# Kernel tuning notes

Measured on AMD Instinct MI355X. Metric: run time of the kernel, lower is better.

Reference implementation:

```python
import jax, jax.numpy as jnp
import numpy as np

MAX_ITER = 10   # float32 branch of cg()
TOL = 1e-10

def _cdot(a, b):
    # complex_dot: sum(conj(a) * b) over all elements
    return jnp.sum(jnp.conj(a) * b)

def _A(p, smaps, mask):
    # p: [H,W] complex, smaps: [C,H,W] complex, mask: [H,W] real
    return jnp.fft.fft2(smaps * p[None], norm='ortho') * mask[None]

def _AH(y, smaps, mask):
    imgs = jnp.fft.ifft2(y * mask[None], norm='ortho')
    return jnp.sum(jnp.conj(smaps) * imgs, axis=0)  # [H,W]

def _cg(M, rhs):
    # conjugate gradient, faithful to the TF while_loop body
    def cond(s):
        i, rTr, x, r, p = s
        return jnp.logical_and(i < MAX_ITER, rTr > TOL)
    def body(s):
        i, rTr, x, r, p = s
        Ap = M(p)
        alpha = rTr / jnp.real(_cdot(p, Ap))
        x = x + p * alpha
        r = r - Ap * alpha
        rTrNew = jnp.real(_cdot(r, r))
        beta = rTrNew / rTr
        p = r + p * beta
        return (i + 1, rTrNew, x, r, p)
    rTr0 = jnp.real(_cdot(rhs, rhs))
    s0 = (jnp.int32(0), rTr0, jnp.zeros_like(rhs), rhs, rhs)
    return jax.lax.while_loop(cond, body, s0)[2]

def _solve_one(lambdaa, rhs, smaps, mask):
    M = lambda p: _AH(_A(p, smaps, mask), smaps, mask) + p * lambdaa
    return _cg(M, rhs)

_solve_b = jax.vmap(_solve_one, in_axes=(None, 0, 0, 0))  # replaces map_fn
_AH_b = jax.vmap(_AH, in_axes=(0, 0, 0))

def setup_inputs():
    key = jax.random.key(0)
    ks = jax.random.split(key, 7)
    B, C, H, W = 4, 16, 384, 384
    f = lambda k, s: jax.random.normal(k, s, dtype=jnp.float32)
    return {
        'lambdaa': 0.05 * jnp.ones((), jnp.float32),
        'x_re': f(ks[0], (B, H, W)),
        'x_im': f(ks[1], (B, H, W)),
        'y_re': f(ks[2], (B, C, H, W)),
        'y_im': f(ks[3], (B, C, H, W)),
        'smaps_re': f(ks[4], (B, C, H, W)),
        'smaps_im': f(ks[5], (B, C, H, W)),
        'mask': (jax.random.uniform(ks[6], (B, H, W)) < 0.33).astype(jnp.float32),
    }

def reference(lambdaa, x_re, x_im, y_re, y_im, smaps_re, smaps_im, mask):
    x = jax.lax.complex(x_re, x_im)
    y = jax.lax.complex(y_re, y_im)
    smaps = jax.lax.complex(smaps_re, smaps_im)
    # rhs = AH(y) + lambdaa * x
    rhs = _AH_b(y, smaps, mask) + x * lambdaa
    out = _solve_b(lambdaa, rhs, smaps, mask)  # [B,H,W] complex
    return jnp.stack([out.real, out.imag], axis=-1)  # [B,H,W,2] float32
```

## Files before the change

kernel.cpp:

```cpp
#include <hip/hip_runtime.h>
#include <hip/hip_fp16.h>


#define Bn 4
#define Cn 16
#define Hn 384
#define Wn 384
#define NPIX (Hn*Wn)
#define NPIX2 (NPIX/2)
#define TPB 256
#define CTPB 512
#define NCOL 16
#define TOLF 1e-10f
#define NITER 10
#define RED_BLKS 72
#define GRP 4
#define CPG 4
#define RPITCH 416
#define CPITCH 417

__device__ __forceinline__ float2 cadd(float2 a, float2 b){ return make_float2(a.x+b.x, a.y+b.y); }
__device__ __forceinline__ float2 csub(float2 a, float2 b){ return make_float2(a.x-b.x, a.y-b.y); }
__device__ __forceinline__ float2 cmulf(float2 a, float2 b){
  return make_float2(a.x*b.x - a.y*b.y, a.x*b.y + a.y*b.x);
}

__device__ __forceinline__ void wave_fence(){ asm volatile("s_waitcnt lgkmcnt(0)" ::: "memory"); }

template<int IMM>
__device__ __forceinline__ float2 shx(float2 v){
  int x = __builtin_amdgcn_ds_swizzle(__float_as_int(v.x), IMM);
  int y = __builtin_amdgcn_ds_swizzle(__float_as_int(v.y), IMM);
  return make_float2(__int_as_float(x), __int_as_float(y));
}

template<int CTRL>
__device__ __forceinline__ float2 dpp2(float2 v){
  int x = __builtin_amdgcn_mov_dpp(__float_as_int(v.x), CTRL, 0xF, 0xF, true);
  int y = __builtin_amdgcn_mov_dpp(__float_as_int(v.y), CTRL, 0xF, 0xF, true);
  return make_float2(__int_as_float(x), __int_as_float(y));
}
__device__ __forceinline__ float2 xchg1 (float2 v){ return dpp2<0xB1>(v);  }
__device__ __forceinline__ float2 xchg2 (float2 v){ return dpp2<0x4E>(v);  }
__device__ __forceinline__ float2 xchg4 (float2 v){ return dpp2<0x1B>(dpp2<0x141>(v)); }
__device__ __forceinline__ float2 xchg8 (float2 v){ return dpp2<0x128>(v); }
__device__ __forceinline__ float2 xchg16(float2 v){ return shx<0x401F>(v); }

__device__ __forceinline__ int rev5(int x){
  return ((x&1)<<4) | ((x&2)<<2) | (x&4) | ((x&8)>>2) | ((x&16)>>4);
}

__device__ __forceinline__ int offmap(int w){ return w + ((w*683)>>13); }

template<int DIR>
__device__ __forceinline__ void fft12(float2* v)
{
  const float S3 = (DIR<0) ? -0.86602540378443864676f : 0.86602540378443864676f;
  const float sg = (DIR<0) ? -1.f : 1.f;
  float2 t[4][3];
#pragma unroll
  for (int b = 0; b < 4; ++b) {
    float2 a0 = v[b], a1 = v[4+b], a2 = v[8+b];
    float2 s = cadd(a1,a2), d = csub(a1,a2);
    float2 mm = make_float2(a0.x - 0.5f*s.x, a0.y - 0.5f*s.y);
    float2 e  = make_float2(-d.y*S3, d.x*S3);
    t[b][0] = cadd(a0,s);
    t[b][1] = cadd(mm,e);
    t[b][2] = csub(mm,e);
  }
  const float2 w1  = make_float2(0.86602540378443864676f, sg*0.5f);
  const float2 w2  = make_float2(0.5f, sg*0.86602540378443864676f);
  const float2 w3  = make_float2(0.f, sg);
  const float2 w4t = make_float2(-0.5f, sg*0.86602540378443864676f);
  const float2 w6  = make_float2(-1.f, 0.f);
  t[1][1] = cmulf(t[1][1], w1);  t[1][2] = cmulf(t[1][2], w2);
  t[2][1] = cmulf(t[2][1], w2);  t[2][2] = cmulf(t[2][2], w4t);
  t[3][1] = cmulf(t[3][1], w3);  t[3][2] = cmulf(t[3][2], w6);
#pragma unroll
  for (int c = 0; c < 3; ++c) {
    float2 e = cadd(t[0][c], t[2][c]);
    float2 f = csub(t[0][c], t[2][c]);
    float2 g = cadd(t[1][c], t[3][c]);
    float2 h = csub(t[1][c], t[3][c]);
    float2 ih = (DIR<0) ? make_float2(h.y, -h.x) : make_float2(-h.y, h.x);
    v[c]   = cadd(e,g);
    v[c+3] = cadd(f,ih);
    v[c+6] = csub(e,g);
    v[c+9] = csub(f,ih);
  }
}

template<int DIR>
__device__ __forceinline__ void fft32_lanes(float2* v, int li)
{
  const float c2pi = (DIR<0) ? -6.2831853071795864769f : 6.2831853071795864769f;
  const float sg   = (DIR<0) ? -1.f : 1.f;
  float s, c;
  __sincosf(c2pi*(1.f/32.f)*(float)(li&15), &s, &c); float2 wA = make_float2(c,s);
  __sincosf(c2pi*(1.f/16.f)*(float)(li&7),  &s, &c); float2 wB = make_float2(c,s);
  __sincosf(c2pi*(1.f/ 8.f)*(float)(li&3),  &s, &c); float2 wC = make_float2(c,s);
  bool bA = li & 16, bB = li & 8, bC = li & 4, bD = li & 2, bE = li & 1;
#pragma unroll
  for (int k = 0; k < 12; ++k) {
    float2 a = v[k], o;
    o = xchg16(a); a = bA ? cmulf(csub(o,a), wA) : cadd(a,o);
    o = xchg8 (a); a = bB ? cmulf(csub(o,a), wB) : cadd(a,o);
    o = xchg4 (a); a = bC ? cmulf(csub(o,a), wC) : cadd(a,o);
    o = xchg2 (a);
    { float2 su = cadd(a,o), d = csub(o,a);
      float2 dw = bE ? make_float2(-sg*d.y, sg*d.x) : d;
      a = bD ? dw : su; }
    o = xchg1 (a); a = bE ? csub(o,a) : cadd(a,o);
    v[k] = a;
  }
}

template<int DIR>
__device__ __forceinline__ void fft32_lanes_dit(float2* v, int li)
{
  const float c2pi = (DIR<0) ? -6.2831853071795864769f : 6.2831853071795864769f;
  const float sg   = (DIR<0) ? -1.f : 1.f;
  float s, c;
  __sincosf(c2pi*(1.f/32.f)*(float)(li&15), &s, &c); float2 wA = make_float2(c,s);
  __sincosf(c2pi*(1.f/16.f)*(float)(li&7),  &s, &c); float2 wB = make_float2(c,s);
  __sincosf(c2pi*(1.f/ 8.f)*(float)(li&3),  &s, &c); float2 wC = make_float2(c,s);
  bool bA = li & 16, bB = li & 8, bC = li & 4, bD = li & 2, bE = li & 1;
#pragma unroll
  for (int k = 0; k < 12; ++k) {
    float2 a = v[k], o;
    o = xchg1(a); a = bE ? csub(o,a) : cadd(a,o);
    { float2 aw = make_float2(-sg*a.y, sg*a.x);
      a = (bD && bE) ? aw : a;
      o = xchg2(a); a = bD ? csub(o,a) : cadd(a,o); }
    { float2 aw = cmulf(a, wC); a = bC ? aw : a;
      o = xchg4(a); a = bC ? csub(o,a) : cadd(a,o); }
    { float2 aw = cmulf(a, wB); a = bB ? aw : a;
      o = xchg8(a); a = bB ? csub(o,a) : cadd(a,o); }
    { float2 aw = cmulf(a, wA); a = bA ? aw : a;
      o = xchg16(a); a = bA ? csub(o,a) : cadd(a,o); }
    v[k] = a;
  }
}

template<int DIR>
__device__ __forceinline__ void fft384(float2* v, int li)
{
  fft12<DIR>(v);
  const float c2pi = (DIR<0) ? -6.2831853071795864769f : 6.2831853071795864769f;
  float s, c;
  __sincosf(c2pi*(1.f/384.f)*(float)li, &s, &c);
  float2 W = make_float2(c,s), cw = W;
#pragma unroll
  for (int k = 1; k < 12; ++k) { v[k] = cmulf(v[k], cw); cw = cmulf(cw, W); }
  fft32_lanes<DIR>(v, li);
}

template<int DIR>
__device__ __forceinline__ void fft384_scr(float2* v, int li)
{
  fft32_lanes_dit<DIR>(v, li);
  const float c2pi = (DIR<0) ? -6.2831853071795864769f : 6.2831853071795864769f;
  float s, c;
  __sincosf(c2pi*(1.f/384.f)*(float)li, &s, &c);
  float2 W = make_float2(c,s), cw = W;
#pragma unroll
  for (int k = 1; k < 12; ++k) { v[k] = cmulf(v[k], cw); cw = cmulf(cw, W); }
  fft12<DIR>(v);
}


template<bool HS>
__global__ __launch_bounds__(TPB) void k_row_fwd(
    const float2* __restrict__ p, const float* __restrict__ Sre,
    const float* __restrict__ Sim, const __half2* __restrict__ Sh,
    __half2* __restrict__ tmp)
{
  int tid = threadIdx.x;
  int wave = tid>>6, lane = tid&63, sub = lane>>5, li = lane&31;
  int row = wave*2 + sub;
  int tile = blockIdx.x % (Hn/8);
  int bc   = blockIdx.x / (Hn/8);
  int b = bc / Cn;
  int h = tile*8 + row;
  size_t gbase = (size_t)bc*NPIX + (size_t)h*Wn;
  size_t pbase = (size_t)b*NPIX + (size_t)h*Wn;

  float2 v[12];
#pragma unroll
  for (int k = 0; k < 12; ++k) {
    int w = 32*k + li;
    float2 pv = p[pbase + w];
    float sr, si;
    if (HS) { float2 sv = __half22float2(Sh[gbase + w]); sr = sv.x; si = sv.y; }
    else    { sr = Sre[gbase + w]; si = Sim[gbase + w]; }
    v[k] = make_float2(sr*pv.x - si*pv.y, sr*pv.y + si*pv.x);
  }
  fft384<-1>(v, li);
#pragma unroll
  for (int k = 0; k < 12; ++k)
    tmp[gbase + 32*k + li] = __float22half2_rn(v[k]);
}

template<bool HS>
__global__ __launch_bounds__(TPB) void k_row_inv_scr(
    const __half2* __restrict__ tmp, const float* __restrict__ Sre,
    const float* __restrict__ Sim, const __half2* __restrict__ Sh,
    float2* __restrict__ partial)
{
  int tid = threadIdx.x;
  int wave = tid>>6, lane = tid&63, sub = lane>>5, li = lane&31;
  int row = wave*2 + sub;
  int tile = blockIdx.x % (Hn/8);
  int rest = blockIdx.x / (Hn/8);
  int g = rest % GRP;
  int b = rest / GRP;
  int h = tile*8 + row;

  size_t gbase0 = ((size_t)b*Cn + g*CPG)*NPIX + (size_t)h*Wn;
  __half2 hb[12];
#pragma unroll
  for (int k = 0; k < 12; ++k) hb[k] = tmp[gbase0 + 32*k + li];

  float2 acc[12];
#pragma unroll
  for (int k = 0; k < 12; ++k) acc[k] = make_float2(0.f, 0.f);

  for (int j = 0; j < CPG; ++j) {
    size_t gb = gbase0 + (size_t)j*NPIX;
    float2 vc[12];
#pragma unroll
    for (int k = 0; k < 12; ++k) vc[k] = __half22float2(hb[k]);
    if (j + 1 < CPG) {
      size_t gbn = gb + NPIX;
#pragma unroll
      for (int k = 0; k < 12; ++k) hb[k] = tmp[gbn + 32*k + li];
    }
    fft384_scr<1>(vc, li);
#pragma unroll
    for (int k = 0; k < 12; ++k) {
      int w = 32*k + li;
      float sr, si;
      if (HS) { float2 sv = __half22float2(Sh[gb + w]); sr = sv.x; si = sv.y; }
      else    { sr = Sre[gb + w]; si = Sim[gb + w]; }
      acc[k].x += sr*vc[k].x + si*vc[k].y;
      acc[k].y += sr*vc[k].y - si*vc[k].x;
    }
  }
  size_t pbase = ((size_t)g*Bn + b)*NPIX + (size_t)h*Wn;
#pragma unroll
  for (int k = 0; k < 12; ++k) partial[pbase + 32*k + li] = acc[k];
}

__global__ __launch_bounds__(TPB) void k_row_inv_nat(
    const __half2* __restrict__ tmp, const float* __restrict__ Sre,
    const float* __restrict__ Sim, float2* __restrict__ partial)
{
  __shared__ float2 lbuf[8*RPITCH];
  int tid = threadIdx.x;
  int wave = tid>>6, lane = tid&63, sub = lane>>5, li = lane&31;
  int row = wave*2 + sub;
  int tile = blockIdx.x % (Hn/8);
  int rest = blockIdx.x / (Hn/8);
  int g = rest % GRP;
  int b = rest / GRP;
  int h = tile*8 + row;
  int m = rev5(li);
  float2* lrow = lbuf + row*RPITCH;

  size_t gbase0 = ((size_t)b*Cn + g*CPG)*NPIX + (size_t)h*Wn;
  __half2 hb[12];
#pragma unroll
  for (int k = 0; k < 12; ++k) hb[k] = tmp[gbase0 + 32*k + li];

  float2 acc[12];
#pragma unroll
  for (int k = 0; k < 12; ++k) acc[k] = make_float2(0.f, 0.f);

  for (int j = 0; j < CPG; ++j) {
    size_t gb = gbase0 + (size_t)j*NPIX;
    float2 vc[12];
#pragma unroll
    for (int k = 0; k < 12; ++k) vc[k] = __half22float2(hb[k]);
    if (j + 1 < CPG) {
      size_t gbn = gb + NPIX;
#pragma unroll
      for (int k = 0; k < 12; ++k) hb[k] = tmp[gbn + 32*k + li];
    }
    fft384<1>(vc, li);
    wave_fence();
#pragma unroll
    for (int k = 0; k < 12; ++k) lrow[13*m + k] = vc[k];
    wave_fence();
#pragma unroll
    for (int k = 0; k < 12; ++k) {
      int w = 32*k + li;
      float2 u = lrow[offmap(w)];
      float sr = Sre[gb + w], si = Sim[gb + w];
      acc[k].x += sr*u.x + si*u.y;
      acc[k].y += sr*u.y - si*u.x;
    }
  }
  size_t pbase = ((size_t)g*Bn + b)*NPIX + (size_t)h*Wn;
#pragma unroll
  for (int k = 0; k < 12; ++k) partial[pbase + 32*k + li] = acc[k];
}

__global__ __launch_bounds__(TPB) void k_spack(
    const float* __restrict__ sre, const float* __restrict__ sim,
    __half2* __restrict__ sh)
{
  size_t i = (size_t)blockIdx.x*TPB + threadIdx.x;
  if (i < (size_t)Bn*Cn*NPIX) sh[i] = __floats2half2_rn(sre[i], sim[i]);
}

__global__ __launch_bounds__(TPB) void k_maskp(
    const float* __restrict__ mask, float* __restrict__ maskP,
    float* __restrict__ scal)
{
  int idx = blockIdx.x*TPB + threadIdx.x;
  if (blockIdx.x == 0) scal[threadIdx.x] = 0.0f;
  if (idx >= Bn*NPIX) return;
  int k = idx % 12; int t = idx / 12;
  int li = t & 31; t >>= 5;
  int wa = t % Wn; int b = t / Wn;
  int wt = (wa >> 5) + 12*rev5(wa & 31);
  maskP[idx] = mask[((size_t)b*Hn + (k + 12*rev5(li)))*Wn + wt] * (1.0f/(float)NPIX);
}

__global__ __launch_bounds__(CTPB) void k_col_full(
    __half2* __restrict__ tmp, const float* __restrict__ maskP)
{
  __shared__ __half2 dbuf[NCOL*CPITCH];
  int tid = threadIdx.x;
  int wave = tid>>6, lane = tid&63, sub = lane>>5, li = lane&31;
  int col = wave*2 + sub;
  int tile = blockIdx.x % (Wn/NCOL);
  int bc   = blockIdx.x / (Wn/NCOL);
  int b = bc / Cn;
  int w0 = tile*NCOL;
  size_t tbase = (size_t)bc*NPIX;

  for (int e = tid; e < NCOL*Hn; e += CTPB) {
    int wi = e & (NCOL-1), h = e >> 4;
    dbuf[wi*CPITCH + offmap(h)] = tmp[tbase + (size_t)h*Wn + w0 + wi];
  }
  __syncthreads();

  __half2* drow = dbuf + col*CPITCH;
  int w = w0 + col;
  const float4* mp4 = (const float4*)(maskP + (((size_t)b*Wn + w)*32 + li)*12);
  float4 m0 = mp4[0], m1 = mp4[1], m2 = mp4[2];
  float2 v[12];
#pragma unroll
  for (int k = 0; k < 12; ++k) v[k] = __half22float2(drow[offmap(32*k + li)]);
  fft384<-1>(v, li);
  float mk[12] = {m0.x,m0.y,m0.z,m0.w, m1.x,m1.y,m1.z,m1.w, m2.x,m2.y,m2.z,m2.w};
#pragma unroll
  for (int k = 0; k < 12; ++k) v[k] = make_float2(v[k].x*mk[k], v[k].y*mk[k]);
  fft384_scr<1>(v, li);
#pragma unroll
  for (int k = 0; k < 12; ++k) drow[offmap(32*k + li)] = __float22half2_rn(v[k]);
  __syncthreads();

  for (int e = tid; e < NCOL*Hn; e += CTPB) {
    int wi = e & (NCOL-1), h = e >> 4;
    tmp[tbase + (size_t)h*Wn + w0 + wi] = dbuf[wi*CPITCH + offmap(h)];
  }
}

__global__ __launch_bounds__(CTPB) void k_col_rhs(
    const float* __restrict__ yre, const float* __restrict__ yim,
    const float* __restrict__ mask, __half2* __restrict__ tmp)
{
  __shared__ float2 dbuf[NCOL*CPITCH];
  int tid = threadIdx.x;
  int wave = tid>>6, lane = tid&63, sub = lane>>5, li = lane&31;
  int col = wave*2 + sub;
  int tile = blockIdx.x % (Wn/NCOL);
  int bc   = blockIdx.x / (Wn/NCOL);
  int b = bc / Cn;
  int w0 = tile*NCOL;
  size_t tbase = (size_t)bc*NPIX;
  size_t mbase = (size_t)b*NPIX;

  for (int e = tid; e < NCOL*Hn; e += CTPB) {
    int wi = e & (NCOL-1), h = e >> 4;
    size_t gi = (size_t)h*Wn + w0 + wi;
    float mv = mask[mbase + gi] * (1.0f/384.0f);
    dbuf[wi*CPITCH + offmap(h)] = make_float2(yre[tbase+gi]*mv, yim[tbase+gi]*mv);
  }
  __syncthreads();

  float2* drow = dbuf + col*CPITCH;
  int m = rev5(li);
  float2 v[12];
#pragma unroll
  for (int k = 0; k < 12; ++k) v[k] = drow[offmap(32*k + li)];
  fft384<1>(v, li);
  wave_fence();
#pragma unroll
  for (int k = 0; k < 12; ++k) drow[13*m + k] = v[k];
  __syncthreads();

  for (int e = tid; e < NCOL*Hn; e += CTPB) {
    int wi = e & (NCOL-1), h = e >> 4;
    tmp[tbase + (size_t)h*Wn + w0 + wi] = __float22half2_rn(dbuf[wi*CPITCH + offmap(h)]);
  }
}


__device__ __forceinline__ void block_reduce_atomic(float sum, float* target)
{
  __shared__ float red[TPB/64];
  for (int off = 32; off > 0; off >>= 1) sum += __shfl_down(sum, off, 64);
  int wv = threadIdx.x >> 6;
  if ((threadIdx.x & 63) == 0) red[wv] = sum;
  __syncthreads();
  if (threadIdx.x == 0) {
    float t = red[0] + red[1] + red[2] + red[3];
    unsafeAtomicAdd(target, t);
  }
  __syncthreads();
}

__global__ __launch_bounds__(TPB) void k_rhs_init(
    const float* __restrict__ xre, const float* __restrict__ xim,
    const float* __restrict__ lam, const float2* __restrict__ partial,
    float2* __restrict__ r, float2* __restrict__ p, float2* __restrict__ x,
    float* __restrict__ scal)
{
  int b = blockIdx.y;
  float l = lam[0];
  float sum = 0.0f;
  const float2* xr2 = (const float2*)(xre + (size_t)b*NPIX);
  const float2* xi2 = (const float2*)(xim + (size_t)b*NPIX);
  float4* r4 = (float4*)(r + (size_t)b*NPIX);
  float4* p4 = (float4*)(p + (size_t)b*NPIX);
  float4* x4 = (float4*)(x + (size_t)b*NPIX);
  for (int i = blockIdx.x*TPB + threadIdx.x; i < NPIX2; i += RED_BLKS*TPB) {
    float2 re = xr2[i], im = xi2[i];
    float4 rv = make_float4(l*re.x, l*im.x, l*re.y, l*im.y);
#pragma unroll
    for (int g = 0; g < GRP; ++g) {
      float4 pv = ((const float4*)(partial + ((size_t)g*Bn + b)*NPIX))[i];
      rv.x += pv.x; rv.y += pv.y; rv.z += pv.z; rv.w += pv.w;
    }
    r4[i] = rv; p4[i] = rv;
    x4[i] = make_float4(0.f, 0.f, 0.f, 0.f);
    sum += rv.x*rv.x + rv.y*rv.y + rv.z*rv.z + rv.w*rv.w;
  }
  block_reduce_atomic(sum, &scal[b]);
}

__global__ __launch_bounds__(TPB) void k_combine_dot3(
    const float2* __restrict__ p, const float2* __restrict__ r,
    const float* __restrict__ lam, const float2* __restrict__ partial,
    float2* __restrict__ Ap, float* __restrict__ slot)
{
  int b = blockIdx.y;
  float l = lam[0];
  float s_pAp = 0.f, s_AA = 0.f, s_rA = 0.f;
  const float4* p4 = (const float4*)(p + (size_t)b*NPIX);
  const float4* r4 = (const float4*)(r + (size_t)b*NPIX);
  float4* A4 = (float4*)(Ap + (size_t)b*NPIX);
  for (int i = blockIdx.x*TPB + threadIdx.x; i < NPIX2; i += RED_BLKS*TPB) {
    float4 pv = p4[i];
    float4 av = make_float4(l*pv.x, l*pv.y, l*pv.z, l*pv.w);
#pragma unroll
    for (int g = 0; g < GRP; ++g) {
      float4 qv = ((const float4*)(partial + ((size_t)g*Bn + b)*NPIX))[i];
      av.x += qv.x; av.y += qv.y; av.z += qv.z; av.w += qv.w;
    }
    A4[i] = av;
    float4 rv = r4[i];
    s_pAp += pv.x*av.x + pv.y*av.y + pv.z*av.z + pv.w*av.w;
    s_AA  += av.x*av.x + av.y*av.y + av.z*av.z + av.w*av.w;
    s_rA  += rv.x*av.x + rv.y*av.y + rv.z*av.z + rv.w*av.w;
  }
  block_reduce_atomic(s_pAp, &slot[b]);
  block_reduce_atomic(s_AA,  &slot[4+b]);
  block_reduce_atomic(s_rA,  &slot[8+b]);
}

__global__ __launch_bounds__(TPB) void k_upd(
    float2* __restrict__ x, float2* __restrict__ r, float2* __restrict__ p,
    const float2* __restrict__ Ap, float* __restrict__ scal, int it)
{
  int b = blockIdx.y;
  float rtr = scal[it*4 + b];
  const float* slot = scal + 64 + it*12;
  bool act = rtr > TOLF;
  float alpha = act ? rtr / slot[b] : 0.f;
  float rtrn = act ? fmaxf(rtr - 2.f*alpha*slot[8+b] + alpha*alpha*slot[4+b], 0.f) : rtr;
  float beta = act ? rtrn / rtr : 0.f;
  if (blockIdx.x == 0 && threadIdx.x == 0) scal[(it+1)*4 + b] = rtrn;
  if (!act) return;
  float4* x4 = (float4*)(x + (size_t)b*NPIX);
  float4* r4 = (float4*)(r + (size_t)b*NPIX);
  float4* p4 = (float4*)(p + (size_t)b*NPIX);
  const float4* A4 = (const float4*)(Ap + (size_t)b*NPIX);
  for (int i = blockIdx.x*TPB + threadIdx.x; i < NPIX2; i += RED_BLKS*TPB) {
    float4 pv = p4[i], av = A4[i], xv = x4[i], rv = r4[i];
    xv.x += alpha*pv.x; xv.y += alpha*pv.y; xv.z += alpha*pv.z; xv.w += alpha*pv.w;
    rv.x -= alpha*av.x; rv.y -= alpha*av.y; rv.z -= alpha*av.z; rv.w -= alpha*av.w;
    x4[i] = xv; r4[i] = rv;
    p4[i] = make_float4(rv.x + beta*pv.x, rv.y + beta*pv.y,
                        rv.z + beta*pv.z, rv.w + beta*pv.w);
  }
}


extern "C" void kernel_launch(void* const* d_in, const int* in_sizes, int n_in,
                              void* d_out, int out_size, void* d_ws, size_t ws_size,
                              hipStream_t stream)
{
  const float* lam  = (const float*)d_in[0];
  const float* xre  = (const float*)d_in[1];
  const float* xim  = (const float*)d_in[2];
  const float* yre  = (const float*)d_in[3];
  const float* yim  = (const float*)d_in[4];
  const float* sre  = (const float*)d_in[5];
  const float* sim  = (const float*)d_in[6];
  const float* mask = (const float*)d_in[7];

  const size_t szTmp  = (size_t)Bn*Cn*NPIX*sizeof(__half2);
  const size_t szVec  = (size_t)Bn*NPIX*sizeof(float2);
  const size_t szMask = (size_t)Bn*NPIX*sizeof(float);
  const size_t szSh   = (size_t)Bn*Cn*NPIX*sizeof(__half2);
  const size_t base   = szTmp + (size_t)GRP*szVec + 3*szVec + 2048 + szMask;
  const bool useSh    = (ws_size >= base + szSh);

  char* ws = (char*)d_ws;
  __half2* tmp = (__half2*)ws;  ws += szTmp;
  float2* part = (float2*)ws;   ws += (size_t)GRP*szVec;
  float2* r    = (float2*)ws;   ws += szVec;
  float2* p    = (float2*)ws;   ws += szVec;
  float2* Ap   = (float2*)ws;   ws += szVec;
  float*  scal = (float*)ws;    ws += 2048;
  float*  mskP = (float*)ws;    ws += szMask;
  __half2* Sh  = (__half2*)ws;
  float2* x    = (float2*)d_out;

  dim3 blk(TPB);
  dim3 rg(RED_BLKS, Bn);
  int grid_row = Bn*Cn*(Hn/8);
  int grid_col = Bn*Cn*(Wn/NCOL);
  int grid_inv = Bn*GRP*(Hn/8);

  k_maskp<<<(Bn*NPIX)/TPB, blk, 0, stream>>>(mask, mskP, scal);
  if (useSh)
    k_spack<<<(Bn*Cn*NPIX)/TPB, blk, 0, stream>>>(sre, sim, Sh);

  k_col_rhs<<<grid_col, CTPB, 0, stream>>>(yre, yim, mask, tmp);
  k_row_inv_nat<<<grid_inv, blk, 0, stream>>>(tmp, sre, sim, part);
  k_rhs_init<<<rg, blk, 0, stream>>>(xre, xim, lam, part, r, p, x, scal);

  for (int it = 0; it < NITER; ++it) {
    if (useSh) {
      k_row_fwd<true><<<grid_row, blk, 0, stream>>>(p, sre, sim, Sh, tmp);
      k_col_full<<<grid_col, CTPB, 0, stream>>>(tmp, mskP);
      k_row_inv_scr<true><<<grid_inv, blk, 0, stream>>>(tmp, sre, sim, Sh, part);
    } else {
      k_row_fwd<false><<<grid_row, blk, 0, stream>>>(p, sre, sim, Sh, tmp);
      k_col_full<<<grid_col, CTPB, 0, stream>>>(tmp, mskP);
      k_row_inv_scr<false><<<grid_inv, blk, 0, stream>>>(tmp, sre, sim, Sh, part);
    }
    k_combine_dot3<<<rg, blk, 0, stream>>>(p, r, lam, part, Ap, scal + 64 + it*12);
    k_upd<<<rg, blk, 0, stream>>>(x, r, p, Ap, scal, it);
  }
}
```

Before: 1.393 ms.

## Fuse CG vector update into next iteration's forward row FFT with ping-pong buffers

Removes the separate k_upd pass by recomputing alpha/beta and applying the r/p/x update inside the forward row FFT kernel of the next iteration, with only channel-0 blocks writing the updated vectors. New r and p go to ping-pong buffers so other channel blocks can still read the old values. A final k_upd_x kernel applies the last x update. In exchange, every channel block now reads Ap, r and p, and the path only runs when the workspace is large enough for the extra buffers.

```diff
diff --git a/kernel.cpp b/kernel.cpp
--- a/kernel.cpp
+++ b/kernel.cpp
@@ -194,6 +194,61 @@
     if (HS) { float2 sv = __half22float2(Sh[gbase + w]); sr = sv.x; si = sv.y; }
     else    { sr = Sre[gbase + w]; si = Sim[gbase + w]; }
     v[k] = make_float2(sr*pv.x - si*pv.y, sr*pv.y + si*pv.x);
+  }
+  fft384<-1>(v, li);
+#pragma unroll
+  for (int k = 0; k < 12; ++k)
+    tmp[gbase + 32*k + li] = __float22half2_rn(v[k]);
+}
+
+template<bool HS>
+__global__ __launch_bounds__(TPB) void k_row_fwd_upd(
+    const float2* __restrict__ pin, const float2* __restrict__ rin,
+    const float2* __restrict__ Ap, float* __restrict__ scal, int uidx,
+    float2* __restrict__ pout, float2* __restrict__ rout,
+    float2* __restrict__ x,
+    const float* __restrict__ Sre, const float* __restrict__ Sim,
+    const __half2* __restrict__ Sh, __half2* __restrict__ tmp)
+{
+  int tid = threadIdx.x;
+  int wave = tid>>6, lane = tid&63, sub = lane>>5, li = lane&31;
+  int row = wave*2 + sub;
+  int tile = blockIdx.x % (Hn/8);
+  int bc   = blockIdx.x / (Hn/8);
+  int b = bc / Cn;
+  int c = bc % Cn;
+  int h = tile*8 + row;
+  size_t gbase = (size_t)bc*NPIX + (size_t)h*Wn;
+  size_t pbase = (size_t)b*NPIX + (size_t)h*Wn;
+
+  float rtr = scal[uidx*4 + b];
+  const float* slot = scal + 64 + uidx*12;
+  bool act = rtr > TOLF;
+  float alpha = act ? rtr / slot[b] : 0.f;
+  float rtrn = act ? fmaxf(rtr - 2.f*alpha*slot[8+b] + alpha*alpha*slot[4+b], 0.f) : rtr;
+  float beta = act ? rtrn / rtr : 0.f;
+  if (c == 0 && tile == 0 && tid == 0) scal[(uidx+1)*4 + b] = rtrn;
+  bool wr = (c == 0);
+
+  float2 v[12];
+#pragma unroll
+  for (int k = 0; k < 12; ++k) {
+    int w = 32*k + li;
+    float2 pv = pin[pbase + w];
+    float2 av = Ap[pbase + w];
+    float2 rv = rin[pbase + w];
+    float2 rn = make_float2(rv.x - alpha*av.x, rv.y - alpha*av.y);
+    float2 pn = act ? make_float2(rn.x + beta*pv.x, rn.y + beta*pv.y) : pv;
+    if (wr) {
+      rout[pbase + w] = rn;
+      pout[pbase + w] = pn;
+      float2 xv = x[pbase + w];
+      x[pbase + w] = make_float2(xv.x + alpha*pv.x, xv.y + alpha*pv.y);
+    }
+    float sr, si;
+    if (HS) { float2 sv = __half22float2(Sh[gbase + w]); sr = sv.x; si = sv.y; }
+    else    { sr = Sre[gbase + w]; si = Sim[gbase + w]; }
+    v[k] = make_float2(sr*pn.x - si*pn.y, sr*pn.y + si*pn.x);
   }
   fft384<-1>(v, li);
 #pragma unroll
@@ -509,6 +564,25 @@
   }
 }
 
+__global__ __launch_bounds__(TPB) void k_upd_x(
+    float2* __restrict__ x, const float2* __restrict__ p,
+    const float* __restrict__ scal, int uidx)
+{
+  int b = blockIdx.y;
+  float rtr = scal[uidx*4 + b];
+  const float* slot = scal + 64 + uidx*12;
+  bool act = rtr > TOLF;
+  if (!act) return;
+  float alpha = rtr / slot[b];
+  float4* x4 = (float4*)(x + (size_t)b*NPIX);
+  const float4* p4 = (const float4*)(p + (size_t)b*NPIX);
+  for (int i = blockIdx.x*TPB + threadIdx.x; i < NPIX2; i += RED_BLKS*TPB) {
+    float4 pv = p4[i], xv = x4[i];
+    x4[i] = make_float4(xv.x + alpha*pv.x, xv.y + alpha*pv.y,
+                        xv.z + alpha*pv.z, xv.w + alpha*pv.w);
+  }
+}
+
 
 extern "C" void kernel_launch(void* const* d_in, const int* in_sizes, int n_in,
                               void* d_out, int out_size, void* d_ws, size_t ws_size,
@@ -529,16 +603,19 @@
   const size_t szSh   = (size_t)Bn*Cn*NPIX*sizeof(__half2);
   const size_t base   = szTmp + (size_t)GRP*szVec + 3*szVec + 2048 + szMask;
   const bool useSh    = (ws_size >= base + szSh);
+  const bool useFused = useSh && (ws_size >= base + szSh + 2*szVec);
 
   char* ws = (char*)d_ws;
   __half2* tmp = (__half2*)ws;  ws += szTmp;
   float2* part = (float2*)ws;   ws += (size_t)GRP*szVec;
-  float2* r    = (float2*)ws;   ws += szVec;
-  float2* p    = (float2*)ws;   ws += szVec;
+  float2* r0   = (float2*)ws;   ws += szVec;
+  float2* p0   = (float2*)ws;   ws += szVec;
   float2* Ap   = (float2*)ws;   ws += szVec;
   float*  scal = (float*)ws;    ws += 2048;
   float*  mskP = (float*)ws;    ws += szMask;
-  __half2* Sh  = (__half2*)ws;
+  __half2* Sh  = (__half2*)ws;  ws += szSh;
+  float2* r1   = (float2*)ws;   ws += szVec;
+  float2* p1   = (float2*)ws;
   float2* x    = (float2*)d_out;
 
   dim3 blk(TPB);
@@ -553,19 +630,39 @@
 
   k_col_rhs<<<grid_col, CTPB, 0, stream>>>(yre, yim, mask, tmp);
   k_row_inv_nat<<<grid_inv, blk, 0, stream>>>(tmp, sre, sim, part);
-  k_rhs_init<<<rg, blk, 0, stream>>>(xre, xim, lam, part, r, p, x, scal);
-
-  for (int it = 0; it < NITER; ++it) {
-    if (useSh) {
-      k_row_fwd<true><<<grid_row, blk, 0, stream>>>(p, sre, sim, Sh, tmp);
+  k_rhs_init<<<rg, blk, 0, stream>>>(xre, xim, lam, part, r0, p0, x, scal);
+
+  if (useFused) {
+    float2* pa[2] = {p0, p1};
+    float2* ra[2] = {r0, r1};
+    k_row_fwd<true><<<grid_row, blk, 0, stream>>>(p0, sre, sim, Sh, tmp);
+    k_col_full<<<grid_col, CTPB, 0, stream>>>(tmp, mskP);
+    k_row_inv_scr<true><<<grid_inv, blk, 0, stream>>>(tmp, sre, sim, Sh, part);
+    k_combine_dot3<<<rg, blk, 0, stream>>>(p0, r0, lam, part, Ap, scal + 64);
+    for (int it = 1; it < NITER; ++it) {
+      float2* pin  = pa[(it-1)&1]; float2* rin  = ra[(it-1)&1];
+      float2* pout = pa[it&1];     float2* rout = ra[it&1];
+      k_row_fwd_upd<true><<<grid_row, blk, 0, stream>>>(
+          pin, rin, Ap, scal, it-1, pout, rout, x, sre, sim, Sh, tmp);
       k_col_full<<<grid_col, CTPB, 0, stream>>>(tmp, mskP);
       k_row_inv_scr<true><<<grid_inv, blk, 0, stream>>>(tmp, sre, sim, Sh, part);
-    } else {
-      k_row_fwd<false><<<grid_row, blk, 0, stream>>>(p, sre, sim, Sh, tmp);
-      k_col_full<<<grid_col, CTPB, 0, stream>>>(tmp, mskP);
-      k_row_inv_scr<false><<<grid_inv, blk, 0, stream>>>(tmp, sre, sim, Sh, part);
-    }
-    k_combine_dot3<<<rg, blk, 0, stream>>>(p, r, lam, part, Ap, scal + 64 + it*12);
-    k_upd<<<rg, blk, 0, stream>>>(x, r, p, Ap, scal, it);
-  }
-}
+      k_combine_dot3<<<rg, blk, 0, stream>>>(pout, rout, lam, part, Ap,
+                                             scal + 64 + it*12);
+    }
+    k_upd_x<<<rg, blk, 0, stream>>>(x, pa[(NITER-1)&1], scal, NITER-1);
+  } else {
+    for (int it = 0; it < NITER; ++it) {
+      if (useSh) {
+        k_row_fwd<true><<<grid_row, blk, 0, stream>>>(p0, sre, sim, Sh, tmp);
+        k_col_full<<<grid_col, CTPB, 0, stream>>>(tmp, mskP);
+        k_row_inv_scr<true><<<grid_inv, blk, 0, stream>>>(tmp, sre, sim, Sh, part);
+      } else {
+        k_row_fwd<false><<<grid_row, blk, 0, stream>>>(p0, sre, sim, Sh, tmp);
+        k_col_full<<<grid_col, CTPB, 0, stream>>>(tmp, mskP);
+        k_row_inv_scr<false><<<grid_inv, blk, 0, stream>>>(tmp, sre, sim, Sh, part);
+      }
+      k_combine_dot3<<<rg, blk, 0, stream>>>(p0, r0, lam, part, Ap, scal + 64 + it*12);
+      k_upd<<<rg, blk, 0, stream>>>(x, r0, p0, Ap, scal, it);
+    }
+  }
+}
```

Result: slower. 1.423 ms (+2.1%).

## Fuse inverse row FFT coil reduction with combine and dot products

Applied to the files above, without the earlier changes.

Adds a kernel that performs the inverse row FFT for all 16 coils of two rows per block, reduces the coil sums in shared memory, adds lambda*p, writes Ap and accumulates the three CG dot products atomically. It replaces the separate partial-sum kernel plus combine kernel on the half-precision smaps path. This removes the partial buffer write and read and one launch per iteration. The cost is a smaller grid (Bn*Hn/2 blocks) with sequential coil loops per chain, which may reduce parallelism, and atomics make the reduction order nondeterministic.

```diff
diff --git a/kernel.cpp b/kernel.cpp
--- a/kernel.cpp
+++ b/kernel.cpp
@@ -199,6 +199,93 @@
 #pragma unroll
   for (int k = 0; k < 12; ++k)
     tmp[gbase + 32*k + li] = __float22half2_rn(v[k]);
+}
+
+template<bool HS>
+__global__ __launch_bounds__(TPB) void k_row_inv_dot(
+    const __half2* __restrict__ tmp, const float* __restrict__ Sre,
+    const float* __restrict__ Sim, const __half2* __restrict__ Sh,
+    const float2* __restrict__ p, const float2* __restrict__ r,
+    const float* __restrict__ lam,
+    float2* __restrict__ Ap, float* __restrict__ slot)
+{
+  __shared__ float2 lred[6][12][32];
+  int tid = threadIdx.x;
+  int wave = tid>>6, lane = tid&63, sub = lane>>5, li = lane&31;
+  int sl = wave*2 + sub;
+  int row = sl & 1, chain = sl >> 1;
+  int tile = blockIdx.x % (Hn/2);
+  int b    = blockIdx.x / (Hn/2);
+  int h = tile*2 + row;
+
+  size_t gbase0 = ((size_t)b*Cn + chain*CPG)*NPIX + (size_t)h*Wn;
+  __half2 hb[12];
+#pragma unroll
+  for (int k = 0; k < 12; ++k) hb[k] = tmp[gbase0 + 32*k + li];
+
+  float2 acc[12];
+#pragma unroll
+  for (int k = 0; k < 12; ++k) acc[k] = make_float2(0.f, 0.f);
+
+  for (int j = 0; j < CPG; ++j) {
+    size_t gb = gbase0 + (size_t)j*NPIX;
+    float2 vc[12];
+#pragma unroll
+    for (int k = 0; k < 12; ++k) vc[k] = __half22float2(hb[k]);
+    if (j + 1 < CPG) {
+      size_t gbn = gb + NPIX;
+#pragma unroll
+      for (int k = 0; k < 12; ++k) hb[k] = tmp[gbn + 32*k + li];
+    }
+    fft384_scr<1>(vc, li);
+#pragma unroll
+    for (int k = 0; k < 12; ++k) {
+      int w = 32*k + li;
+      float sr, si;
+      if (HS) { float2 sv = __half22float2(Sh[gb + w]); sr = sv.x; si = sv.y; }
+      else    { sr = Sre[gb + w]; si = Sim[gb + w]; }
+      acc[k].x += sr*vc[k].x + si*vc[k].y;
+      acc[k].y += sr*vc[k].y - si*vc[k].x;
+    }
+  }
+
+  if (chain > 0) {
+#pragma unroll
+    for (int k = 0; k < 12; ++k) lred[(chain-1)*2 + row][k][li] = acc[k];
+  }
+  __syncthreads();
+  if (chain == 0) {
+#pragma unroll
+    for (int q = 0; q < 3; ++q)
+#pragma unroll
+      for (int k = 0; k < 12; ++k) {
+        float2 t = lred[q*2 + row][k][li];
+        acc[k].x += t.x; acc[k].y += t.y;
+      }
+    float l = lam[0];
+    size_t pb = (size_t)b*NPIX + (size_t)h*Wn;
+    float s_pAp = 0.f, s_AA = 0.f, s_rA = 0.f;
+#pragma unroll
+    for (int k = 0; k < 12; ++k) {
+      int w = 32*k + li;
+      float2 pv = p[pb + w], rv = r[pb + w];
+      float2 av = make_float2(l*pv.x + acc[k].x, l*pv.y + acc[k].y);
+      Ap[pb + w] = av;
+      s_pAp += pv.x*av.x + pv.y*av.y;
+      s_AA  += av.x*av.x + av.y*av.y;
+      s_rA  += rv.x*av.x + rv.y*av.y;
+    }
+    for (int off = 32; off > 0; off >>= 1) {
+      s_pAp += __shfl_down(s_pAp, off, 64);
+      s_AA  += __shfl_down(s_AA , off, 64);
+      s_rA  += __shfl_down(s_rA , off, 64);
+    }
+    if (lane == 0) {
+      unsafeAtomicAdd(&slot[b],   s_pAp);
+      unsafeAtomicAdd(&slot[4+b], s_AA);
+      unsafeAtomicAdd(&slot[8+b], s_rA);
+    }
+  }
 }
 
 template<bool HS>
@@ -543,9 +630,10 @@
 
   dim3 blk(TPB);
   dim3 rg(RED_BLKS, Bn);
-  int grid_row = Bn*Cn*(Hn/8);
-  int grid_col = Bn*Cn*(Wn/NCOL);
-  int grid_inv = Bn*GRP*(Hn/8);
+  int grid_row  = Bn*Cn*(Hn/8);
+  int grid_col  = Bn*Cn*(Wn/NCOL);
+  int grid_inv  = Bn*GRP*(Hn/8);
+  int grid_invd = Bn*(Hn/2);
 
   k_maskp<<<(Bn*NPIX)/TPB, blk, 0, stream>>>(mask, mskP, scal);
   if (useSh)
@@ -559,13 +647,14 @@
     if (useSh) {
       k_row_fwd<true><<<grid_row, blk, 0, stream>>>(p, sre, sim, Sh, tmp);
       k_col_full<<<grid_col, CTPB, 0, stream>>>(tmp, mskP);
-      k_row_inv_scr<true><<<grid_inv, blk, 0, stream>>>(tmp, sre, sim, Sh, part);
+      k_row_inv_dot<true><<<grid_invd, blk, 0, stream>>>(
+          tmp, sre, sim, Sh, p, r, lam, Ap, scal + 64 + it*12);
     } else {
       k_row_fwd<false><<<grid_row, blk, 0, stream>>>(p, sre, sim, Sh, tmp);
       k_col_full<<<grid_col, CTPB, 0, stream>>>(tmp, mskP);
       k_row_inv_scr<false><<<grid_inv, blk, 0, stream>>>(tmp, sre, sim, Sh, part);
-    }
-    k_combine_dot3<<<rg, blk, 0, stream>>>(p, r, lam, part, Ap, scal + 64 + it*12);
+      k_combine_dot3<<<rg, blk, 0, stream>>>(p, r, lam, part, Ap, scal + 64 + it*12);
+    }
     k_upd<<<rg, blk, 0, stream>>>(x, r, p, Ap, scal, it);
   }
 }
```

Result: no change. 1.398 ms (+0.4%).
